# Kernel tuning notes

Measured on AMD Instinct MI355X. Metric: run time of the kernel, lower is better.

## Reference

```python
import jax, jax.numpy as jnp
import numpy as np

THRESHOLD = 0.5
EPS = 1e-6


def setup_inputs() -> dict:
    key = jax.random.key(0)
    k1, k2, k3 = jax.random.split(key, 3)
    B, C, T = 32, 6, 64
    K, N = 8, 128
    S, P = 32, 64
    points = jax.random.normal(k1, (B, C, T, 2), dtype=jnp.float32)
    road_boundary = jax.random.normal(k2, (B, K, N, 2), dtype=jnp.float32)
    centerlines = jax.random.normal(k3, (B, S, P, 2), dtype=jnp.float32)
    return {"points": points, "road_boundary": road_boundary, "centerlines": centerlines}


def _cross(v1, v2):
    return v1[..., 0] * v2[..., 1] - v1[..., 1] * v2[..., 0]


def reference(points, road_boundary, centerlines):
    B, C, T, _ = points.shape
    _, K, N, _ = road_boundary.shape
    _, S, P, _ = centerlines.shape

    # --- min distance to boundary segments ---
    seg_a = road_boundary[:, :, :-1, :]          # (B,K,N-1,2)
    seg_d = road_boundary[:, :, 1:, :] - seg_a   # (B,K,N-1,2)

    p = points[:, None, :, :, None, :]           # (B,1,C,T,1,2)
    a = seg_a[:, :, None, None, :, :]            # (B,K,1,1,N-1,2)
    d = seg_d[:, :, None, None, :, :]            # (B,K,1,1,N-1,2)

    v1 = p - a                                   # (B,K,C,T,N-1,2)
    dot = (v1 * d).sum(-1)                       # (B,K,C,T,N-1)
    edge_sq = (d * d).sum(-1)                    # (B,K,1,1,N-1)
    proj = jnp.clip(dot / (edge_sq + EPS), 0.0, 1.0)
    closest = a + d * proj[..., None]            # (B,K,C,T,N-1,2)
    dist = jnp.sqrt(((p - closest) ** 2).sum(-1))  # (B,K,C,T,N-1)
    min_dist = dist.min(axis=-1).min(axis=1)     # (B,C,T)

    # --- nearest centerline point ---
    cl = centerlines.reshape(B, S * P, 2)        # (B,SP,2)
    v2 = points[:, None, :, :, :] - cl[:, :, None, None, :]  # (B,SP,C,T,2)
    cl_dist_sq = (v2 ** 2).sum(-1)               # (B,SP,C,T)
    idx = jnp.argmin(cl_dist_sq, axis=1)         # (B,C,T)
    closest_cl = cl[jnp.arange(B)[:, None, None], idx]  # (B,C,T,2)

    # --- segment intersection test: (point -> nearest centerline pt) vs boundary edges ---
    a1 = points[:, None, None, :, :, :]          # (B,1,1,C,T,2)
    a2 = closest_cl[:, None, None, :, :, :]      # (B,1,1,C,T,2)
    b1 = seg_a[:, :, :, None, None, :]           # (B,K,N-1,1,1,2)
    db = seg_d[:, :, :, None, None, :]           # (B,K,N-1,1,1,2)

    da = a2 - a1
    dp = a1 - b1                                 # (B,K,N-1,C,T,2)
    dadb = _cross(da, db)                        # (B,K,N-1,C,T)
    t = _cross(da, dp) / (dadb + EPS)
    u = _cross(db, dp) / (dadb + EPS)
    intersect = (t >= 0.0) & (t <= 1.0) & (u >= 0.0) & (u <= 1.0)

    inside = ~jnp.any(intersect, axis=(1, 2))    # (B,C,T)
    min_dist = jnp.where(inside, -min_dist, min_dist)
    return jax.nn.relu(min_dist + THRESHOLD).sum(-1)  # (B,C)
```

## Files before the change

### kernel.cpp

```cpp
#include <hip/hip_runtime.h>

constexpr int cB = 32, cC = 6, cT = 64;
constexpr int cK = 8, cN = 128;
constexpr int cS = 32, cP = 64;
constexpr int NSEG_PAD = cK * cN;
constexpr int NCL  = cS * cP;
constexpr int G = 8;
constexpr int LPP = 32;
constexpr float F_EPS = 1e-6f;
constexpr float F_THRESHOLD = 0.5f;

__global__ __launch_bounds__(256, 8) void offroad_kernel(
    const float* __restrict__ points,
    const float* __restrict__ road_boundary,
    const float* __restrict__ centerlines,
    float* __restrict__ out)
{
    const int blk = blockIdx.x;
    const int g  = blk & (G - 1);
    const int bc = blk >> 3;
    const int b  = bc / cC;
    const int tid = threadIdx.x;

    const float2* __restrict__ rb2 =
        (const float2*)(road_boundary + (size_t)b * cK * cN * 2);
    const float4* __restrict__ cl4 =
        (const float4*)(centerlines + (size_t)b * NCL * 2);

    const int t = (g << 3) | (tid >> 5);
    const int q = tid & (LPP - 1);
    const size_t pbase = (((size_t)bc) * cT + t) * 2;
    const float px = points[pbase + 0];
    const float py = points[pbase + 1];

    float min_d2  = 3.4e38f;
    float best_d2 = 3.4e38f;
    int   best_i  = 0x7fffffff;
    #pragma unroll 4
    for (int i = 0; i < NSEG_PAD / LPP; ++i) {
        const int s = q + i * LPP;
        const int n = s & (cN - 1);
        const int s1 = s + ((n < cN - 1) ? 1 : 0);
        float2 a  = rb2[s];
        float2 nx = rb2[s1];
        float dx = nx.x - a.x, dy = nx.y - a.y;
        float v1x = px - a.x,  v1y = py - a.y;
        float dot = v1x * dx + v1y * dy;
        float e2  = dx * dx + dy * dy + F_EPS;
        float proj = dot * __builtin_amdgcn_rcpf(e2);
        proj = fminf(fmaxf(proj, 0.0f), 1.0f);
        float ex = v1x - dx * proj;
        float ey = v1y - dy * proj;
        min_d2 = fminf(min_d2, ex * ex + ey * ey);

        float4 cp = cl4[s];
        float dxa = px - cp.x, dya = py - cp.y;
        float d2a = dxa * dxa + dya * dya;
        float dxb = px - cp.z, dyb = py - cp.w;
        float d2b = dxb * dxb + dyb * dyb;
        int   ia = 2 * s;
        float dmin = d2a; int imin = ia;
        if (d2b < d2a) { dmin = d2b; imin = ia + 1; }
        if (dmin < best_d2 || (dmin == best_d2 && imin < best_i)) {
            best_d2 = dmin; best_i = imin;
        }
    }
    #pragma unroll
    for (int off = 1; off <= 16; off <<= 1) {
        float od2 = __shfl_xor(best_d2, off);
        int   oi  = __shfl_xor(best_i, off);
        if (od2 < best_d2 || (od2 == best_d2 && oi < best_i)) {
            best_d2 = od2; best_i = oi;
        }
    }
    const float2 cc = ((const float2*)cl4)[best_i];

    const float dax = cc.x - px, day = cc.y - py;
    int hit = 0;
    #pragma unroll 4
    for (int i = 0; i < NSEG_PAD / LPP; ++i) {
        const int s = q + i * LPP;
        const int n = s & (cN - 1);
        const int s1 = s + ((n < cN - 1) ? 1 : 0);
        float2 a  = rb2[s];
        float2 nx = rb2[s1];
        float dbx = nx.x - a.x, dby = nx.y - a.y;
        float dpx = px - a.x,   dpy = py - a.y;
        float dadb = dax * dby - day * dbx;
        float inv = __builtin_amdgcn_rcpf(dadb + F_EPS);
        float tt = (dax * dpy - day * dpx) * inv;
        float uu = (dbx * dpy - dby * dpx) * inv;
        bool inb = (tt >= 0.0f) & (tt <= 1.0f) & (uu >= 0.0f) & (uu <= 1.0f);
        hit |= (int)((n < cN - 1) & inb);
    }

    #pragma unroll
    for (int off = 1; off <= 16; off <<= 1) {
        min_d2 = fminf(min_d2, __shfl_xor(min_d2, off));
        hit |= __shfl_xor(hit, off);
    }

    float md = sqrtf(min_d2);
    float sd = hit ? md : -md;
    float val = fmaxf(sd + F_THRESHOLD, 0.0f);
    if (q != 0) val = 0.0f;

    #pragma unroll
    for (int off = 32; off >= 1; off >>= 1)
        val += __shfl_down(val, off);
    if ((tid & 63) == 0)
        atomicAdd(&out[bc], val);
}

extern "C" void kernel_launch(void* const* d_in, const int* in_sizes, int n_in,
                              void* d_out, int out_size, void* d_ws, size_t ws_size,
                              hipStream_t stream) {
    const float* points      = (const float*)d_in[0];
    const float* boundary    = (const float*)d_in[1];
    const float* centerlines = (const float*)d_in[2];
    float* out = (float*)d_out;
    hipMemsetAsync(out, 0, (size_t)out_size * sizeof(float), stream);
    offroad_kernel<<<cB * cC * G, 256, 0, stream>>>(points, boundary, centerlines, out);
}
```

Measured before the change: 98.69 us.

## Process four points per wavefront to reuse segment and centerline loads

```diff
diff --git a/kernel.cpp b/kernel.cpp
--- a/kernel.cpp
+++ b/kernel.cpp
@@ -5,111 +5,137 @@
 constexpr int cS = 32, cP = 64;
 constexpr int NSEG_PAD = cK * cN;
 constexpr int NCL  = cS * cP;
-constexpr int G = 8;
-constexpr int LPP = 32;
+constexpr int G = 4;
+constexpr int PPW = 4;
 constexpr float F_EPS = 1e-6f;
 constexpr float F_THRESHOLD = 0.5f;
 
-__global__ __launch_bounds__(256, 8) void offroad_kernel(
+__global__ __launch_bounds__(256) void offroad_kernel(
     const float* __restrict__ points,
     const float* __restrict__ road_boundary,
     const float* __restrict__ centerlines,
     float* __restrict__ out)
 {
-    const int blk = blockIdx.x;
-    const int g  = blk & (G - 1);
-    const int bc = blk >> 3;
-    const int b  = bc / cC;
-    const int tid = threadIdx.x;
+    const int blk  = blockIdx.x;
+    const int g    = blk & (G - 1);
+    const int bc   = blk >> 2;
+    const int b    = bc / cC;
+    const int lane = threadIdx.x & 63;
+    const int wave = threadIdx.x >> 6;
 
     const float2* __restrict__ rb2 =
         (const float2*)(road_boundary + (size_t)b * cK * cN * 2);
     const float4* __restrict__ cl4 =
         (const float4*)(centerlines + (size_t)b * NCL * 2);
 
-    const int t = (g << 3) | (tid >> 5);
-    const int q = tid & (LPP - 1);
-    const size_t pbase = (((size_t)bc) * cT + t) * 2;
-    const float px = points[pbase + 0];
-    const float py = points[pbase + 1];
+    const int t0 = (g << 4) | (wave << 2);
+    const float* pb = points + (((size_t)bc) * cT + t0) * 2;
+    float px[PPW], py[PPW];
+    #pragma unroll
+    for (int p = 0; p < PPW; ++p) { px[p] = pb[2 * p]; py[p] = pb[2 * p + 1]; }
 
-    float min_d2  = 3.4e38f;
-    float best_d2 = 3.4e38f;
-    int   best_i  = 0x7fffffff;
-    #pragma unroll 4
-    for (int i = 0; i < NSEG_PAD / LPP; ++i) {
-        const int s = q + i * LPP;
+    float min_d2[PPW], best_d2[PPW];
+    int   best_i[PPW];
+    #pragma unroll
+    for (int p = 0; p < PPW; ++p) {
+        min_d2[p] = 3.4e38f; best_d2[p] = 3.4e38f; best_i[p] = 0x7fffffff;
+    }
+
+    #pragma unroll 2
+    for (int i = 0; i < NSEG_PAD / 64; ++i) {
+        const int s = lane + (i << 6);
         const int n = s & (cN - 1);
         const int s1 = s + ((n < cN - 1) ? 1 : 0);
-        float2 a  = rb2[s];
-        float2 nx = rb2[s1];
-        float dx = nx.x - a.x, dy = nx.y - a.y;
-        float v1x = px - a.x,  v1y = py - a.y;
-        float dot = v1x * dx + v1y * dy;
-        float e2  = dx * dx + dy * dy + F_EPS;
-        float proj = dot * __builtin_amdgcn_rcpf(e2);
-        proj = fminf(fmaxf(proj, 0.0f), 1.0f);
-        float ex = v1x - dx * proj;
-        float ey = v1y - dy * proj;
-        min_d2 = fminf(min_d2, ex * ex + ey * ey);
+        const float2 a  = rb2[s];
+        const float2 nx = rb2[s1];
+        const float4 cp = cl4[s];
+        const float dx = nx.x - a.x, dy = nx.y - a.y;
+        const float inv_e2 = __builtin_amdgcn_rcpf(dx * dx + dy * dy + F_EPS);
+        const int ia = 2 * s;
 
-        float4 cp = cl4[s];
-        float dxa = px - cp.x, dya = py - cp.y;
-        float d2a = dxa * dxa + dya * dya;
-        float dxb = px - cp.z, dyb = py - cp.w;
-        float d2b = dxb * dxb + dyb * dyb;
-        int   ia = 2 * s;
-        float dmin = d2a; int imin = ia;
-        if (d2b < d2a) { dmin = d2b; imin = ia + 1; }
-        if (dmin < best_d2 || (dmin == best_d2 && imin < best_i)) {
-            best_d2 = dmin; best_i = imin;
+        #pragma unroll
+        for (int p = 0; p < PPW; ++p) {
+            float v1x = px[p] - a.x, v1y = py[p] - a.y;
+            float proj = (v1x * dx + v1y * dy) * inv_e2;
+            proj = fminf(fmaxf(proj, 0.0f), 1.0f);
+            float ex = v1x - dx * proj;
+            float ey = v1y - dy * proj;
+            min_d2[p] = fminf(min_d2[p], ex * ex + ey * ey);
+
+            float dxa = px[p] - cp.x, dya = py[p] - cp.y;
+            float d2a = dxa * dxa + dya * dya;
+            float dxb = px[p] - cp.z, dyb = py[p] - cp.w;
+            float d2b = dxb * dxb + dyb * dyb;
+            float dmin = d2a; int imin = ia;
+            if (d2b < d2a) { dmin = d2b; imin = ia + 1; }
+            if (dmin < best_d2[p] ||
+                (dmin == best_d2[p] && imin < best_i[p])) {
+                best_d2[p] = dmin; best_i[p] = imin;
+            }
         }
-    }
-    #pragma unroll
-    for (int off = 1; off <= 16; off <<= 1) {
-        float od2 = __shfl_xor(best_d2, off);
-        int   oi  = __shfl_xor(best_i, off);
-        if (od2 < best_d2 || (od2 == best_d2 && oi < best_i)) {
-            best_d2 = od2; best_i = oi;
-        }
-    }
-    const float2 cc = ((const float2*)cl4)[best_i];
-
-    const float dax = cc.x - px, day = cc.y - py;
-    int hit = 0;
-    #pragma unroll 4
-    for (int i = 0; i < NSEG_PAD / LPP; ++i) {
-        const int s = q + i * LPP;
-        const int n = s & (cN - 1);
-        const int s1 = s + ((n < cN - 1) ? 1 : 0);
-        float2 a  = rb2[s];
-        float2 nx = rb2[s1];
-        float dbx = nx.x - a.x, dby = nx.y - a.y;
-        float dpx = px - a.x,   dpy = py - a.y;
-        float dadb = dax * dby - day * dbx;
-        float inv = __builtin_amdgcn_rcpf(dadb + F_EPS);
-        float tt = (dax * dpy - day * dpx) * inv;
-        float uu = (dbx * dpy - dby * dpx) * inv;
-        bool inb = (tt >= 0.0f) & (tt <= 1.0f) & (uu >= 0.0f) & (uu <= 1.0f);
-        hit |= (int)((n < cN - 1) & inb);
     }
 
     #pragma unroll
-    for (int off = 1; off <= 16; off <<= 1) {
-        min_d2 = fminf(min_d2, __shfl_xor(min_d2, off));
-        hit |= __shfl_xor(hit, off);
+    for (int off = 1; off <= 32; off <<= 1) {
+        #pragma unroll
+        for (int p = 0; p < PPW; ++p) {
+            float od2 = __shfl_xor(best_d2[p], off);
+            int   oi  = __shfl_xor(best_i[p], off);
+            if (od2 < best_d2[p] || (od2 == best_d2[p] && oi < best_i[p])) {
+                best_d2[p] = od2; best_i[p] = oi;
+            }
+        }
     }
 
-    float md = sqrtf(min_d2);
-    float sd = hit ? md : -md;
-    float val = fmaxf(sd + F_THRESHOLD, 0.0f);
-    if (q != 0) val = 0.0f;
+    const float2* __restrict__ cl2 = (const float2*)cl4;
+    float dax[PPW], day[PPW];
+    #pragma unroll
+    for (int p = 0; p < PPW; ++p) {
+        float2 cc = cl2[best_i[p]];
+        dax[p] = cc.x - px[p]; day[p] = cc.y - py[p];
+    }
+
+    int hit[PPW] = {0, 0, 0, 0};
+    #pragma unroll 2
+    for (int i = 0; i < NSEG_PAD / 64; ++i) {
+        const int s = lane + (i << 6);
+        const int n = s & (cN - 1);
+        const int s1 = s + ((n < cN - 1) ? 1 : 0);
+        const float2 a  = rb2[s];
+        const float2 nx = rb2[s1];
+        const float dbx = nx.x - a.x, dby = nx.y - a.y;
+        const int valid = (n < cN - 1) ? 1 : 0;
+
+        #pragma unroll
+        for (int p = 0; p < PPW; ++p) {
+            float dpx = px[p] - a.x, dpy = py[p] - a.y;
+            float dadb = dax[p] * dby - day[p] * dbx;
+            float inv = __builtin_amdgcn_rcpf(dadb + F_EPS);
+            float tt = (dax[p] * dpy - day[p] * dpx) * inv;
+            float uu = (dbx * dpy - dby * dpx) * inv;
+            bool inb = (tt >= 0.0f) & (tt <= 1.0f) & (uu >= 0.0f) & (uu <= 1.0f);
+            hit[p] |= valid & (int)inb;
+        }
+    }
 
     #pragma unroll
-    for (int off = 32; off >= 1; off >>= 1)
-        val += __shfl_down(val, off);
-    if ((tid & 63) == 0)
-        atomicAdd(&out[bc], val);
+    for (int off = 1; off <= 32; off <<= 1) {
+        #pragma unroll
+        for (int p = 0; p < PPW; ++p) {
+            min_d2[p] = fminf(min_d2[p], __shfl_xor(min_d2[p], off));
+            hit[p]   |= __shfl_xor(hit[p], off);
+        }
+    }
+
+    float total = 0.0f;
+    #pragma unroll
+    for (int p = 0; p < PPW; ++p) {
+        float md = sqrtf(min_d2[p]);
+        float sd = hit[p] ? md : -md;
+        total += fmaxf(sd + F_THRESHOLD, 0.0f);
+    }
+    if (lane == 0)
+        atomicAdd(&out[bc], total);
 }
 
 extern "C" void kernel_launch(void* const* d_in, const int* in_sizes, int n_in,
```

New measurement: 82.94 us. -16.0%, faster.

## Restructure to one block per (b,c) with lanes as points and waves splitting segments

Applied to the files above, without the earlier changes.

```diff
diff --git a/kernel.cpp b/kernel.cpp
--- a/kernel.cpp
+++ b/kernel.cpp
@@ -3,113 +3,109 @@
 constexpr int cB = 32, cC = 6, cT = 64;
 constexpr int cK = 8, cN = 128;
 constexpr int cS = 32, cP = 64;
-constexpr int NSEG_PAD = cK * cN;
-constexpr int NCL  = cS * cP;
-constexpr int G = 8;
-constexpr int LPP = 32;
+constexpr int NCL = cS * cP;
+constexpr int NW  = 16;
 constexpr float F_EPS = 1e-6f;
 constexpr float F_THRESHOLD = 0.5f;
 
-__global__ __launch_bounds__(256, 8) void offroad_kernel(
+__global__ __launch_bounds__(1024) void offroad_kernel(
     const float* __restrict__ points,
     const float* __restrict__ road_boundary,
     const float* __restrict__ centerlines,
     float* __restrict__ out)
 {
-    const int blk = blockIdx.x;
-    const int g  = blk & (G - 1);
-    const int bc = blk >> 3;
-    const int b  = bc / cC;
-    const int tid = threadIdx.x;
+    __shared__ float s_f[NW][cT];
+    __shared__ int   s_i[NW][cT];
+
+    const int bc   = blockIdx.x;
+    const int b    = bc / cC;
+    const int tid  = threadIdx.x;
+    const int lane = tid & 63;
+    const int wv   = tid >> 6;
+
+    const float2* __restrict__ pts2 =
+        (const float2*)(points + (size_t)bc * cT * 2);
+    const float2 pt = pts2[lane];
+    const float px = pt.x, py = pt.y;
 
     const float2* __restrict__ rb2 =
         (const float2*)(road_boundary + (size_t)b * cK * cN * 2);
     const float4* __restrict__ cl4 =
         (const float4*)(centerlines + (size_t)b * NCL * 2);
+    const float2* __restrict__ cl2 = (const float2*)cl4;
 
-    const int t = (g << 3) | (tid >> 5);
-    const int q = tid & (LPP - 1);
-    const size_t pbase = (((size_t)bc) * cT + t) * 2;
-    const float px = points[pbase + 0];
-    const float py = points[pbase + 1];
-
-    float min_d2  = 3.4e38f;
-    float best_d2 = 3.4e38f;
-    int   best_i  = 0x7fffffff;
+    float bd = 3.4e38f; int bi = 0x7fffffff;
+    const int j0 = wv * (NCL / 2 / NW);
     #pragma unroll 4
-    for (int i = 0; i < NSEG_PAD / LPP; ++i) {
-        const int s = q + i * LPP;
-        const int n = s & (cN - 1);
-        const int s1 = s + ((n < cN - 1) ? 1 : 0);
-        float2 a  = rb2[s];
-        float2 nx = rb2[s1];
-        float dx = nx.x - a.x, dy = nx.y - a.y;
-        float v1x = px - a.x,  v1y = py - a.y;
-        float dot = v1x * dx + v1y * dy;
-        float e2  = dx * dx + dy * dy + F_EPS;
-        float proj = dot * __builtin_amdgcn_rcpf(e2);
-        proj = fminf(fmaxf(proj, 0.0f), 1.0f);
-        float ex = v1x - dx * proj;
-        float ey = v1y - dy * proj;
-        min_d2 = fminf(min_d2, ex * ex + ey * ey);
-
-        float4 cp = cl4[s];
+    for (int jj = 0; jj < NCL / 2 / NW; ++jj) {
+        const int jf = j0 + jj;
+        const float4 cp = cl4[jf];
         float dxa = px - cp.x, dya = py - cp.y;
         float d2a = dxa * dxa + dya * dya;
         float dxb = px - cp.z, dyb = py - cp.w;
         float d2b = dxb * dxb + dyb * dyb;
-        int   ia = 2 * s;
+        const int ia = 2 * jf;
         float dmin = d2a; int imin = ia;
         if (d2b < d2a) { dmin = d2b; imin = ia + 1; }
-        if (dmin < best_d2 || (dmin == best_d2 && imin < best_i)) {
-            best_d2 = dmin; best_i = imin;
-        }
+        if (dmin < bd) { bd = dmin; bi = imin; }
     }
+    s_f[wv][lane] = bd; s_i[wv][lane] = bi;
+    __syncthreads();
+    bd = s_f[0][lane]; bi = s_i[0][lane];
     #pragma unroll
-    for (int off = 1; off <= 16; off <<= 1) {
-        float od2 = __shfl_xor(best_d2, off);
-        int   oi  = __shfl_xor(best_i, off);
-        if (od2 < best_d2 || (od2 == best_d2 && oi < best_i)) {
-            best_d2 = od2; best_i = oi;
-        }
+    for (int w2 = 1; w2 < NW; ++w2) {
+        float od = s_f[w2][lane]; int oi = s_i[w2][lane];
+        if (od < bd || (od == bd && oi < bi)) { bd = od; bi = oi; }
     }
-    const float2 cc = ((const float2*)cl4)[best_i];
+    const float2 cc = cl2[bi];
+    const float dax = cc.x - px, day = cc.y - py;
+    __syncthreads();
 
-    const float dax = cc.x - px, day = cc.y - py;
-    int hit = 0;
+    float mind2 = 3.4e38f; int hit = 0;
+    const int k  = wv >> 1;
+    const int n0 = (wv & 1) ? 64 : 0;
+    const float2* __restrict__ rbv = rb2 + k * cN;
     #pragma unroll 4
-    for (int i = 0; i < NSEG_PAD / LPP; ++i) {
-        const int s = q + i * LPP;
-        const int n = s & (cN - 1);
-        const int s1 = s + ((n < cN - 1) ? 1 : 0);
-        float2 a  = rb2[s];
-        float2 nx = rb2[s1];
-        float dbx = nx.x - a.x, dby = nx.y - a.y;
-        float dpx = px - a.x,   dpy = py - a.y;
-        float dadb = dax * dby - day * dbx;
-        float inv = __builtin_amdgcn_rcpf(dadb + F_EPS);
-        float tt = (dax * dpy - day * dpx) * inv;
-        float uu = (dbx * dpy - dby * dpx) * inv;
-        bool inb = (tt >= 0.0f) & (tt <= 1.0f) & (uu >= 0.0f) & (uu <= 1.0f);
-        hit |= (int)((n < cN - 1) & inb);
+    for (int jj = 0; jj < 64; ++jj) {
+        const int n  = n0 + jj;
+        const int ok = (n < cN - 1) ? 1 : 0;
+        const int nl = ok ? n : (cN - 2);
+        const float2 a = rbv[nl];
+        const float2 e = rbv[nl + 1];
+        const float dx = e.x - a.x, dy = e.y - a.y;
+        const float inv_e2 = __builtin_amdgcn_rcpf(dx * dx + dy * dy + F_EPS);
+        float v1x = px - a.x, v1y = py - a.y;
+        float proj = (v1x * dx + v1y * dy) * inv_e2;
+        proj = __builtin_amdgcn_fmed3f(proj, 0.0f, 1.0f);
+        float ex = v1x - dx * proj;
+        float ey = v1y - dy * proj;
+        mind2 = fminf(mind2, ex * ex + ey * ey);
+        float w   = dax * dy - day * dx + F_EPS;
+        float w2s = w * w;
+        float ct  = (dax * v1y - day * v1x) * w;
+        float cu  = (dx * v1y - dy * v1x) * w;
+        bool inb = (ct >= 0.0f) & (ct <= w2s) & (cu >= 0.0f) & (cu <= w2s);
+        hit |= ok & (int)inb;
     }
 
-    #pragma unroll
-    for (int off = 1; off <= 16; off <<= 1) {
-        min_d2 = fminf(min_d2, __shfl_xor(min_d2, off));
-        hit |= __shfl_xor(hit, off);
+    s_f[wv][lane] = mind2; s_i[wv][lane] = hit;
+    __syncthreads();
+
+    if (wv == 0) {
+        float m = s_f[0][lane]; int h = s_i[0][lane];
+        #pragma unroll
+        for (int w2 = 1; w2 < NW; ++w2) {
+            m = fminf(m, s_f[w2][lane]);
+            h |= s_i[w2][lane];
+        }
+        float md  = sqrtf(m);
+        float val = fmaxf((h ? md : -md) + F_THRESHOLD, 0.0f);
+        #pragma unroll
+        for (int off = 32; off >= 1; off >>= 1)
+            val += __shfl_down(val, off);
+        if (lane == 0)
+            out[bc] = val;
     }
-
-    float md = sqrtf(min_d2);
-    float sd = hit ? md : -md;
-    float val = fmaxf(sd + F_THRESHOLD, 0.0f);
-    if (q != 0) val = 0.0f;
-
-    #pragma unroll
-    for (int off = 32; off >= 1; off >>= 1)
-        val += __shfl_down(val, off);
-    if ((tid & 63) == 0)
-        atomicAdd(&out[bc], val);
 }
 
 extern "C" void kernel_launch(void* const* d_in, const int* in_sizes, int n_in,
@@ -119,6 +115,5 @@
     const float* boundary    = (const float*)d_in[1];
     const float* centerlines = (const float*)d_in[2];
     float* out = (float*)d_out;
-    hipMemsetAsync(out, 0, (size_t)out_size * sizeof(float), stream);
-    offroad_kernel<<<cB * cC * G, 256, 0, stream>>>(points, boundary, centerlines, out);
+    offroad_kernel<<<cB * cC, 1024, 0, stream>>>(points, boundary, centerlines, out);
 }
```

After: 83.18 us. 15.7% less time.
